# Optimization experiments

Hardware: AMD Instinct MI355X
Metric: run time of the kernel (lower is better)

Reference implementation:

```python
import jax, jax.numpy as jnp
import numpy as np

DIM = 512; DEPTH = 2; HEADS = 8; DIM_HEAD = 64; INNER = HEADS * DIM_HEAD
MEM = 16; TOPK = 8; FF = 4 * DIM
NUM_BUCKETS = 32; MAX_DIST = 128
EPS = 1e-5


def _layernorm(x, g, b):
    m = jnp.mean(x, axis=-1, keepdims=True)
    v = jnp.var(x, axis=-1, keepdims=True)
    return (x - m) * jax.lax.rsqrt(v + EPS) * g + b


def _rel_bucket(rel_pos):
    # T5 relative-position bucketing, causal=True (as hardcoded in Encoder)
    num_buckets = NUM_BUCKETS // 2  # 16
    n = -rel_pos
    ret = (n < 0).astype(jnp.int32) * num_buckets
    n = jnp.abs(n)
    max_exact = num_buckets // 2  # 8
    is_small = n < max_exact
    nf = jnp.maximum(n, 1).astype(jnp.float32)  # safe log; masked by is_small where n==0
    val_if_large = max_exact + (
        jnp.log(nf / max_exact) / np.log(MAX_DIST / max_exact) * (num_buckets - max_exact)
    ).astype(jnp.int32)
    val_if_large = jnp.minimum(val_if_large, num_buckets - 1)
    return ret + jnp.where(is_small, n, val_if_large)


def setup_inputs() -> dict:
    key = jax.random.key(0)
    ks = jax.random.split(key, 16)
    B, N = 2, 2048
    w = lambda k, shape, s=0.02: jax.random.normal(k, shape, jnp.float32) * s
    return {
        "x": jax.random.normal(ks[0], (B, N, DIM), jnp.float32),
        "ln1_g": jnp.ones((DEPTH, DIM), jnp.float32),
        "ln1_b": jnp.zeros((DEPTH, DIM), jnp.float32),
        "Wq": w(ks[1], (DEPTH, DIM, INNER)),
        "Wkv": w(ks[2], (DEPTH, DIM, 2 * INNER)),
        "Wo": w(ks[3], (DEPTH, INNER, DIM)),
        "bo": jnp.zeros((DEPTH, DIM), jnp.float32),
        "pre_proj": w(ks[4], (DEPTH, HEADS, HEADS), 1.0),  # torch.randn init
        "mem_k": w(ks[5], (DEPTH, HEADS, MEM, DIM_HEAD), 1.0),
        "mem_v": w(ks[6], (DEPTH, HEADS, MEM, DIM_HEAD), 1.0),
        "ln2_g": jnp.ones((DEPTH, DIM), jnp.float32),
        "ln2_b": jnp.zeros((DEPTH, DIM), jnp.float32),
        "W1": w(ks[7], (DEPTH, DIM, FF)),
        "b1": jnp.zeros((DEPTH, FF), jnp.float32),
        "W2": w(ks[8], (DEPTH, FF, DIM)),
        "b2": jnp.zeros((DEPTH, DIM), jnp.float32),
        "rel_emb": w(ks[9], (NUM_BUCKETS, HEADS)),
    }


def reference(x, ln1_g, ln1_b, Wq, Wkv, Wo, bo, pre_proj, mem_k, mem_v,
              ln2_g, ln2_b, W1, b1, W2, b2, rel_emb):
    B, N, _ = x.shape
    J = N + MEM  # keys include num_mem_kv memory slots
    scale = DIM_HEAD ** -0.5
    # relative position bias, shape (1, H, N, J); same for every layer
    rel = jnp.arange(J)[None, :] - jnp.arange(N)[:, None]
    bias = jnp.transpose(rel_emb[_rel_bucket(rel)], (2, 0, 1))[None]

    for l in range(DEPTH):
        # --- PreNorm(Attention) + residual ---
        h = _layernorm(x, ln1_g[l], ln1_b[l])
        q = (h @ Wq[l]).reshape(B, N, HEADS, DIM_HEAD).transpose(0, 2, 1, 3)
        k, v = jnp.split(h @ Wkv[l], 2, axis=-1)
        k = k.reshape(B, N, HEADS, DIM_HEAD).transpose(0, 2, 1, 3)
        v = v.reshape(B, N, HEADS, DIM_HEAD).transpose(0, 2, 1, 3)
        k = jnp.concatenate([jnp.broadcast_to(mem_k[l], (B, HEADS, MEM, DIM_HEAD)), k], axis=2)
        v = jnp.concatenate([jnp.broadcast_to(mem_v[l], (B, HEADS, MEM, DIM_HEAD)), v], axis=2)
        dots = jnp.einsum('bhid,bhjd->bhij', q, k) * scale
        dots = jnp.einsum('bhij,hk->bkij', dots, pre_proj[l])  # talking heads (pre-softmax)
        dots = dots + bias
        # sparse top-k masking: keep only values >= k-th largest per row
        thr = jax.lax.top_k(dots, TOPK)[0][..., -1:]
        dots = jnp.where(dots < thr, -jnp.inf, dots)
        attn = jax.nn.softmax(dots, axis=-1)
        out = jnp.einsum('bhij,bhjd->bhid', attn, v)
        out = out.transpose(0, 2, 1, 3).reshape(B, N, INNER)
        x = out @ Wo[l] + bo[l] + x
        # --- PreNorm(FeedForward) + residual ---
        h2 = _layernorm(x, ln2_g[l], ln2_b[l])
        x = jax.nn.gelu(h2 @ W1[l] + b1[l], approximate=False) @ W2[l] + b2[l] + x
    return x
```

## Files before the change

### kernel.cpp

```cpp
#include <hip/hip_runtime.h>
#include <cmath>

typedef __bf16 bf16;
typedef __attribute__((ext_vector_type(8))) __bf16 bf16x8;
typedef __attribute__((ext_vector_type(4))) __bf16 bf16x4;
typedef __attribute__((ext_vector_type(4))) float f32x4;

#define NB 2
#define NSEQ 2048
#define NDIM 512
#define NHEADS 8
#define DHEAD 64
#define NMEM 16
#define NJ 2064
#define NJP 2176
#define NFF 2048
#define NROWS (NB*NSEQ)
#define TBL 4111

enum { EPI_QKV = 0, EPI_GELUSPLIT = 1, EPI_RESID = 2 };

template<int BM, int BN, int WAVES_M, int WAVES_N, int EPI>
__global__ __launch_bounds__(256)
void gemm_split(const bf16* __restrict__ A, const bf16* __restrict__ B,
                void* __restrict__ Cv, const float* __restrict__ bias,
                void* __restrict__ Cv2, void* __restrict__ Cv3,
                int K, int lda, int ldb, int ldc, int loA, int loB)
{
  constexpr int BK = 32;
  constexpr int WM = BM / WAVES_M;
  constexpr int WN = BN / WAVES_N;
  constexpr int MF = WM / 16;
  constexpr int NF = WN / 16;
  constexpr int AI = (BM * BK * 2) / 4096;
  constexpr int BI = (BN * BK * 2) / 4096;
  __shared__ bf16 Ash[2][BM * BK];
  __shared__ bf16 Asl[2][BM * BK];
  __shared__ bf16 Bsh[2][BN * BK];
  __shared__ bf16 Bsl[2][BN * BK];

  const int bm0 = blockIdx.x * BM;
  const int bn0 = blockIdx.y * BN;
  const int t = threadIdx.x;
  const int wave = t >> 6, lane = t & 63;
  const int wr = wave / WAVES_N, wc = wave % WAVES_N;
  const int sr = t >> 2, sc = t & 3;
  const int frow = lane & 15, fk = (lane >> 4) * 8;

  auto stage = [&](int buf, int k0) {
#pragma unroll
    for (int qi = 0; qi < AI; ++qi) {
      const long long ro = (long long)(bm0 + qi * 64 + sr) * lda + (k0 + sc * 8);
      __builtin_amdgcn_global_load_lds(
          (const __attribute__((address_space(1))) void*)(A + ro),
          (__attribute__((address_space(3))) void*)(&Ash[buf][qi * 2048 + wave * 512]), 16, 0, 0);
      __builtin_amdgcn_global_load_lds(
          (const __attribute__((address_space(1))) void*)(A + ro + loA),
          (__attribute__((address_space(3))) void*)(&Asl[buf][qi * 2048 + wave * 512]), 16, 0, 0);
    }
#pragma unroll
    for (int qi = 0; qi < BI; ++qi) {
      const long long ro = (long long)(bn0 + qi * 64 + sr) * ldb + (k0 + sc * 8);
      __builtin_amdgcn_global_load_lds(
          (const __attribute__((address_space(1))) void*)(B + ro),
          (__attribute__((address_space(3))) void*)(&Bsh[buf][qi * 2048 + wave * 512]), 16, 0, 0);
      __builtin_amdgcn_global_load_lds(
          (const __attribute__((address_space(1))) void*)(B + ro + loB),
          (__attribute__((address_space(3))) void*)(&Bsl[buf][qi * 2048 + wave * 512]), 16, 0, 0);
    }
  };

  f32x4 acc[MF][NF] = {};

  stage(0, 0);
  __syncthreads();
  int cur = 0;
  for (int k0 = 0; k0 < K; k0 += BK) {
    if (k0 + BK < K) stage(cur ^ 1, k0 + BK);
    bf16x8 afh[MF], afl[MF], bfh[NF], bfl[NF];
#pragma unroll
    for (int m = 0; m < MF; m++) {
      afh[m] = *(const bf16x8*)(&Ash[cur][(wr * WM + m * 16 + frow) * BK + fk]);
      afl[m] = *(const bf16x8*)(&Asl[cur][(wr * WM + m * 16 + frow) * BK + fk]);
    }
#pragma unroll
    for (int n = 0; n < NF; n++) {
      bfh[n] = *(const bf16x8*)(&Bsh[cur][(wc * WN + n * 16 + frow) * BK + fk]);
      bfl[n] = *(const bf16x8*)(&Bsl[cur][(wc * WN + n * 16 + frow) * BK + fk]);
    }
#pragma unroll
    for (int m = 0; m < MF; m++)
#pragma unroll
      for (int n = 0; n < NF; n++) {
        acc[m][n] = __builtin_amdgcn_mfma_f32_16x16x32_bf16(afh[m], bfh[n], acc[m][n], 0, 0, 0);
        acc[m][n] = __builtin_amdgcn_mfma_f32_16x16x32_bf16(afl[m], bfh[n], acc[m][n], 0, 0, 0);
        acc[m][n] = __builtin_amdgcn_mfma_f32_16x16x32_bf16(afh[m], bfl[n], acc[m][n], 0, 0, 0);
      }
    __syncthreads();
    cur ^= 1;
  }

#pragma unroll
  for (int m = 0; m < MF; m++) {
#pragma unroll
    for (int n = 0; n < NF; n++) {
      const int row0 = bm0 + wr * WM + m * 16 + (lane >> 4) * 4;
      const int col = bn0 + wc * WN + n * 16 + (lane & 15);
#pragma unroll
      for (int r = 0; r < 4; r++) {
        const float v = acc[m][n][r];
        const long long i = row0 + r;
        if (EPI == EPI_QKV) {
          const int bb = (int)(i >> 11);
          const int il = (int)(i & 2047);
          if (col < NDIM) {
            const float vq = v * 0.125f;
            bf16* base = (bf16*)Cv;
            const long long ih = i * (long long)(2 * NDIM) + col;
            bf16 h = (bf16)vq;
            base[ih] = h;
            base[ih + NDIM] = (bf16)(vq - (float)h);
          } else if (col < 2 * NDIM) {
            bf16* ks = (bf16*)Cv3;
            const long long ih = ((long long)bb * NJP + il + NMEM) * (long long)(2 * NDIM)
                               + (col - NDIM);
            bf16 h = (bf16)v;
            ks[ih] = h;
            ks[ih + NDIM] = (bf16)(v - (float)h);
          } else {
            ((float*)Cv2)[i * (long long)NDIM + (col - 2 * NDIM)] = v;
          }
        } else if (EPI == EPI_GELUSPLIT) {
          float u = v + bias[col];
          float gl = 0.5f * u * (1.0f + erff(u * 0.7071067811865476f));
          const long long ih = i * (long long)(2 * ldc) + col;
          bf16 h = (bf16)gl;
          ((bf16*)Cv)[ih] = h;
          ((bf16*)Cv)[ih + ldc] = (bf16)(gl - (float)h);
        } else {
          float* xp = ((float*)Cv) + i * ldc + col;
          *xp = *xp + v + bias[col];
        }
      }
    }
  }
}

__global__ __launch_bounds__(256)
void s_gemm_direct(const bf16* __restrict__ Qs, const bf16* __restrict__ Ks,
                   float* __restrict__ S)
{
  const int h = blockIdx.z;
  const int bm0 = blockIdx.x * 128;
  const int bn0 = blockIdx.y * 128;
  const int t = threadIdx.x;
  const int wave = t >> 6, lane = t & 63;
  const int wr = wave >> 1, wc = wave & 1;
  const int frow = lane & 15, fk = (lane >> 4) * 8;

  bf16x8 ah[4][2], al[4][2];
#pragma unroll
  for (int m = 0; m < 4; m++)
#pragma unroll
    for (int kk = 0; kk < 2; kk++) {
      const bf16* ap = Qs + (long long)(bm0 + wr * 64 + m * 16 + frow) * 1024
                     + h * 64 + kk * 32 + fk;
      ah[m][kk] = *(const bf16x8*)(ap);
      al[m][kk] = *(const bf16x8*)(ap + 512);
    }

  f32x4 acc[4][4] = {};
#pragma unroll
  for (int n = 0; n < 4; n++) {
    bf16x8 bh[2], bl[2];
#pragma unroll
    for (int kk = 0; kk < 2; kk++) {
      const bf16* bp = Ks + (long long)(bn0 + wc * 64 + n * 16 + frow) * 1024
                     + h * 64 + kk * 32 + fk;
      bh[kk] = *(const bf16x8*)(bp);
      bl[kk] = *(const bf16x8*)(bp + 512);
    }
#pragma unroll
    for (int m = 0; m < 4; m++)
#pragma unroll
      for (int kk = 0; kk < 2; kk++) {
        acc[m][n] = __builtin_amdgcn_mfma_f32_16x16x32_bf16(ah[m][kk], bh[kk], acc[m][n], 0, 0, 0);
        acc[m][n] = __builtin_amdgcn_mfma_f32_16x16x32_bf16(al[m][kk], bh[kk], acc[m][n], 0, 0, 0);
        acc[m][n] = __builtin_amdgcn_mfma_f32_16x16x32_bf16(ah[m][kk], bl[kk], acc[m][n], 0, 0, 0);
      }
  }

#pragma unroll
  for (int m = 0; m < 4; m++) {
#pragma unroll
    for (int n = 0; n < 4; n++) {
      const int row0 = bm0 + wr * 64 + m * 16 + (lane >> 4) * 4;
      const int col = bn0 + wc * 64 + n * 16 + (lane & 15);
#pragma unroll
      for (int r = 0; r < 4; r++)
        S[(long long)(row0 + r) * (NHEADS * NJP) + h * NJP + col] = acc[m][n][r];
    }
  }
}

__global__ __launch_bounds__(256)
void ln_kernel(const float* __restrict__ x, const float* __restrict__ g,
               const float* __restrict__ b, bf16* __restrict__ out)
{
  const int row = blockIdx.x * 4 + (threadIdx.x >> 6);
  const int lane = threadIdx.x & 63;
  const float* xr = x + (long long)row * NDIM;
  float4 a0 = ((const float4*)xr)[lane];
  float4 a1 = ((const float4*)xr)[lane + 64];
  float s = a0.x + a0.y + a0.z + a0.w + a1.x + a1.y + a1.z + a1.w;
  float ss = a0.x * a0.x + a0.y * a0.y + a0.z * a0.z + a0.w * a0.w
           + a1.x * a1.x + a1.y * a1.y + a1.z * a1.z + a1.w * a1.w;
#pragma unroll
  for (int d = 1; d < 64; d <<= 1) {
    s += __shfl_xor(s, d, 64);
    ss += __shfl_xor(ss, d, 64);
  }
  const float mean = s * (1.0f / NDIM);
  const float var = ss * (1.0f / NDIM) - mean * mean;
  const float rs = rsqrtf(var + 1e-5f);
  float4 g0 = ((const float4*)g)[lane], g1 = ((const float4*)g)[lane + 64];
  float4 b0 = ((const float4*)b)[lane], b1 = ((const float4*)b)[lane + 64];
  bf16* orow = out + (long long)row * (2 * NDIM);
  float y[8] = {
    (a0.x - mean) * rs * g0.x + b0.x, (a0.y - mean) * rs * g0.y + b0.y,
    (a0.z - mean) * rs * g0.z + b0.z, (a0.w - mean) * rs * g0.w + b0.w,
    (a1.x - mean) * rs * g1.x + b1.x, (a1.y - mean) * rs * g1.y + b1.y,
    (a1.z - mean) * rs * g1.z + b1.z, (a1.w - mean) * rs * g1.w + b1.w };
  bf16x4 h0, h1, l0, l1;
#pragma unroll
  for (int j = 0; j < 4; j++) {
    bf16 h = (bf16)y[j];      h0[j] = h;  l0[j] = (bf16)(y[j] - (float)h);
    bf16 h2 = (bf16)y[4 + j]; h1[j] = h2; l1[j] = (bf16)(y[4 + j] - (float)h2);
  }
  *(bf16x4*)(orow + lane * 4) = h0;
  *(bf16x4*)(orow + 256 + lane * 4) = h1;
  *(bf16x4*)(orow + 512 + lane * 4) = l0;
  *(bf16x4*)(orow + 768 + lane * 4) = l1;
}

__global__ __launch_bounds__(256)
void ks_edges(const float* __restrict__ mem_k_l, bf16* __restrict__ Ks)
{
  const int idx = blockIdx.x * 256 + threadIdx.x;
  const int c = idx & 511;
  const int jj = (idx >> 9) & 127;
  const int bb = idx >> 16;
  const int j = (jj < NMEM) ? jj : (jj - NMEM + NJ);
  float kval = 0.f;
  if (jj < NMEM) kval = mem_k_l[((c >> 6) * NMEM + jj) * DHEAD + (c & 63)];
  bf16 hv = (bf16)kval;
  const long long ro = ((long long)bb * NJP + j) * (2 * NDIM) + c;
  Ks[ro] = hv;
  Ks[ro + NDIM] = (bf16)(kval - (float)hv);
}

__global__ __launch_bounds__(512)
void mix_topk_gather(const float* __restrict__ S, const float* __restrict__ kvV,
                     const float* __restrict__ mem_v_l, const float* __restrict__ pp,
                     const float* __restrict__ table2, bf16* __restrict__ obufs,
                     int b)
{
  const int i = blockIdx.x;
  const int k = threadIdx.x >> 6;
  const int lane = threadIdx.x & 63;
  const float* srow = S + (long long)i * (NHEADS * NJP);

  float pk[8];
#pragma unroll
  for (int h = 0; h < 8; h++) pk[h] = pp[h * 8 + k];
  const float* t2k = table2 + k * TBL + (2047 - i);

  float v[34];
#pragma unroll
  for (int t = 0; t < 8; t++) {
    const int j0 = 256 * t + 4 * lane;
    v[4 * t + 0] = t2k[j0];
    v[4 * t + 1] = t2k[j0 + 1];
    v[4 * t + 2] = t2k[j0 + 2];
    v[4 * t + 3] = t2k[j0 + 3];
  }
  {
    const int j0 = 2048 + 2 * lane;
    const int jc = j0 < 2062 ? j0 : 2062;
    v[32] = t2k[jc];
    v[33] = t2k[jc + 1];
  }

#pragma unroll
  for (int h = 0; h < 8; h++) {
    const float* sp = srow + h * NJP;
    const float w = pk[h];
#pragma unroll
    for (int t = 0; t < 8; t++) {
      const float4 s4 = *(const float4*)(sp + 256 * t + 4 * lane);
      v[4 * t + 0] = fmaf(s4.x, w, v[4 * t + 0]);
      v[4 * t + 1] = fmaf(s4.y, w, v[4 * t + 1]);
      v[4 * t + 2] = fmaf(s4.z, w, v[4 * t + 2]);
      v[4 * t + 3] = fmaf(s4.w, w, v[4 * t + 3]);
    }
    const float2 s2 = *(const float2*)(sp + 2048 + 2 * lane);
    v[32] = fmaf(s2.x, w, v[32]);
    v[33] = fmaf(s2.y, w, v[33]);
  }
  {
    const int j0 = 2048 + 2 * lane;
    if (j0 >= NJ) v[32] = -1e30f;
    if (j0 + 1 >= NJ) v[33] = -1e30f;
  }

  float t8[8];
#pragma unroll
  for (int m = 0; m < 8; m++) t8[m] = -3.0e38f;
#pragma unroll
  for (int e = 0; e < 34; e++) {
    float x = v[e];
#pragma unroll
    for (int m = 0; m < 8; m++) {
      const float hi = fmaxf(t8[m], x);
      x = fminf(t8[m], x);
      t8[m] = hi;
    }
  }

#pragma unroll
  for (int d = 1; d < 64; d <<= 1) {
    float o[8], m8[8];
#pragma unroll
    for (int m = 0; m < 8; m++) o[m] = __shfl_xor(t8[m], d, 64);
#pragma unroll
    for (int m = 0; m < 8; m++) m8[m] = fmaxf(t8[m], o[7 - m]);
#define CX(a, bq) { float hi = fmaxf(m8[a], m8[bq]); float lo = fminf(m8[a], m8[bq]); m8[a] = hi; m8[bq] = lo; }
    CX(0, 4) CX(1, 5) CX(2, 6) CX(3, 7)
    CX(0, 2) CX(1, 3) CX(4, 6) CX(5, 7)
    CX(0, 1) CX(2, 3) CX(4, 5) CX(6, 7)
#undef CX
#pragma unroll
    for (int m = 0; m < 8; m++) t8[m] = m8[m];
  }
  const float mx = t8[0];
  const float thr = t8[7];
  float denom = 0.f;
#pragma unroll
  for (int m = 0; m < 8; m++) denom += __expf(t8[m] - mx);
  const float inv = 1.0f / denom;

  float acc = 0.f;
#pragma unroll
  for (int t = 0; t < 8; t++) {
#pragma unroll
    for (int e = 0; e < 4; e++) {
      unsigned long long mball = __ballot(v[t * 4 + e] >= thr);
      while (mball) {
        const int l = __builtin_ctzll(mball);
        mball &= mball - 1;
        const int jj = 256 * t + 4 * l + e;
        const float sv = __shfl(v[t * 4 + e], l);
        const float w = __expf(sv - mx) * inv;
        const float vv = (jj < NMEM)
            ? mem_v_l[(k * NMEM + jj) * DHEAD + lane]
            : kvV[(long long)(b * NSEQ + (jj - NMEM)) * NDIM + k * DHEAD + lane];
        acc = fmaf(w, vv, acc);
      }
    }
  }
#pragma unroll
  for (int e = 0; e < 2; e++) {
    unsigned long long mball = __ballot(v[32 + e] >= thr);
    while (mball) {
      const int l = __builtin_ctzll(mball);
      mball &= mball - 1;
      const int jj = 2048 + 2 * l + e;
      const float sv = __shfl(v[32 + e], l);
      const float w = __expf(sv - mx) * inv;
      const float vv = (jj < NMEM)
          ? mem_v_l[(k * NMEM + jj) * DHEAD + lane]
          : kvV[(long long)(b * NSEQ + (jj - NMEM)) * NDIM + k * DHEAD + lane];
      acc = fmaf(w, vv, acc);
    }
  }

  const long long orow = (long long)(b * NSEQ + i) * (2 * NDIM) + k * DHEAD + lane;
  bf16 h = (bf16)acc;
  obufs[orow] = h;
  obufs[orow + NDIM] = (bf16)(acc - (float)h);
}

__global__ __launch_bounds__(256)
void transpose_split(const float* __restrict__ in, bf16* __restrict__ out,
                     int R, int C)
{
  const long long idx = (long long)blockIdx.x * 256 + threadIdx.x;
  if (idx >= (long long)R * C) return;
  const int r = (int)(idx / C);
  const int c = (int)(idx % C);
  float v = in[idx];
  bf16 h = (bf16)v;
  out[(long long)c * (2 * R) + r] = h;
  out[(long long)c * (2 * R) + R + r] = (bf16)(v - (float)h);
}

__global__ __launch_bounds__(256)
void build_bias2(const float* __restrict__ rel_emb, float* __restrict__ table2)
{
  const int idx = blockIdx.x * 256 + threadIdx.x;
  if (idx >= 8 * TBL) return;
  const int k = idx / TBL;
  const int rel = (idx % TBL) - 2047;
  const int n = -rel;
  const int ret = (n < 0) ? 16 : 0;
  const int na = n < 0 ? -n : n;
  int bucket;
  if (na < 8) {
    bucket = ret + na;
  } else {
    int vl = 8 + (int)(log2((double)na * 0.125) * 2.0);
    vl = vl < 15 ? vl : 15;
    bucket = ret + vl;
  }
  table2[idx] = rel_emb[bucket * 8 + k];
}

extern "C" void kernel_launch(void* const* d_in, const int* in_sizes, int n_in,
                              void* d_out, int out_size, void* d_ws, size_t ws_size,
                              hipStream_t stream)
{
  const float* x_in    = (const float*)d_in[0];
  const float* ln1_g   = (const float*)d_in[1];
  const float* ln1_b   = (const float*)d_in[2];
  const float* Wq      = (const float*)d_in[3];
  const float* Wkv     = (const float*)d_in[4];
  const float* Wo      = (const float*)d_in[5];
  const float* bo      = (const float*)d_in[6];
  const float* pre_proj= (const float*)d_in[7];
  const float* mem_k   = (const float*)d_in[8];
  const float* mem_v   = (const float*)d_in[9];
  const float* ln2_g   = (const float*)d_in[10];
  const float* ln2_b   = (const float*)d_in[11];
  const float* W1      = (const float*)d_in[12];
  const float* b1      = (const float*)d_in[13];
  const float* W2      = (const float*)d_in[14];
  const float* b2      = (const float*)d_in[15];
  const float* rel_emb = (const float*)d_in[16];

  char* p = (char*)d_ws;
  auto alloc = [&](size_t bytes) -> char* {
    char* r = p;
    p += (bytes + 255) & ~(size_t)255;
    return r;
  };

  float* x    = (float*)alloc((size_t)NROWS * NDIM * 4);
  char*  RA   = alloc((size_t)NROWS * 2 * NDIM * 2);
  bf16*  hs    = (bf16*)RA;
  bf16*  obufs = (bf16*)RA;
  char*  RB   = alloc((size_t)NROWS * 2 * NFF * 2);
  bf16*  Qs    = (bf16*)RB;
  bf16*  Ks    = (bf16*)(RB + (size_t)NROWS * 2 * NDIM * 2);
  bf16*  tbufs = (bf16*)RB;
  float* kvV  = (float*)alloc((size_t)NROWS * NDIM * 4);
  float* S    = (float*)alloc((size_t)NSEQ * NHEADS * NJP * 4);
  bf16*  WqkvT= (bf16*)alloc((size_t)2 * 3 * NDIM * 2 * NDIM * 2);
  bf16*  WoT  = (bf16*)alloc((size_t)2 * NDIM * 2 * NDIM * 2);
  bf16*  W1T  = (bf16*)alloc((size_t)2 * NFF * 2 * NDIM * 2);
  bf16*  W2T  = (bf16*)alloc((size_t)2 * NDIM * 2 * NFF * 2);
  float* table2= (float*)alloc((size_t)8 * TBL * 4);

  hipMemcpyAsync(x, x_in, (size_t)NROWS * NDIM * 4, hipMemcpyDeviceToDevice, stream);
  build_bias2<<<(8 * TBL + 255) / 256, 256, 0, stream>>>(rel_emb, table2);
  for (int l = 0; l < 2; l++) {
    bf16* WqkvT_l = WqkvT + (size_t)l * 3 * NDIM * 2 * NDIM;
    transpose_split<<<(NDIM * NDIM + 255) / 256, 256, 0, stream>>>(
        Wq + (size_t)l * NDIM * NDIM, WqkvT_l, NDIM, NDIM);
    transpose_split<<<(2 * NDIM * NDIM + 255) / 256, 256, 0, stream>>>(
        Wkv + (size_t)l * NDIM * 2 * NDIM, WqkvT_l + (size_t)NDIM * 2 * NDIM,
        NDIM, 2 * NDIM);
    transpose_split<<<(NDIM * NDIM + 255) / 256, 256, 0, stream>>>(
        Wo + (size_t)l * NDIM * NDIM, WoT + (size_t)l * NDIM * 2 * NDIM, NDIM, NDIM);
    transpose_split<<<(NDIM * NFF + 255) / 256, 256, 0, stream>>>(
        W1 + (size_t)l * NDIM * NFF, W1T + (size_t)l * NFF * 2 * NDIM, NDIM, NFF);
    transpose_split<<<(NFF * NDIM + 255) / 256, 256, 0, stream>>>(
        W2 + (size_t)l * NFF * NDIM, W2T + (size_t)l * NDIM * 2 * NFF, NFF, NDIM);
  }

  for (int l = 0; l < 2; l++) {
    const bf16* WqkvT_l = WqkvT + (size_t)l * 3 * NDIM * 2 * NDIM;
    const bf16* WoT_l  = WoT + (size_t)l * NDIM * 2 * NDIM;
    const bf16* W1T_l  = W1T + (size_t)l * NFF * 2 * NDIM;
    const bf16* W2T_l  = W2T + (size_t)l * NDIM * 2 * NFF;
    const float* mem_v_l = mem_v + (size_t)l * NHEADS * NMEM * DHEAD;

    ln_kernel<<<NROWS / 4, 256, 0, stream>>>(x, ln1_g + l * NDIM, ln1_b + l * NDIM, hs);
    gemm_split<128, 128, 2, 2, EPI_QKV><<<dim3(NROWS / 128, 12), 256, 0, stream>>>(
        hs, WqkvT_l, Qs, nullptr, kvV, Ks, NDIM, 2 * NDIM, 2 * NDIM, 0, NDIM, NDIM);
    ks_edges<<<(2 * 128 * 512) / 256, 256, 0, stream>>>(
        mem_k + (size_t)l * NHEADS * NMEM * DHEAD, Ks);

    for (int b = 0; b < NB; b++) {
      s_gemm_direct<<<dim3(NSEQ / 128, NJP / 128, NHEADS), 256, 0, stream>>>(
          Qs + (long long)b * NSEQ * 1024, Ks + (long long)b * NJP * 1024, S);
      mix_topk_gather<<<NSEQ, 512, 0, stream>>>(
          S, kvV, mem_v_l, pre_proj + l * 64, table2, obufs, b);
    }

    gemm_split<128, 64, 2, 2, EPI_RESID><<<dim3(NROWS / 128, NDIM / 64), 256, 0, stream>>>(
        obufs, WoT_l, x, bo + l * NDIM, nullptr, nullptr,
        NDIM, 2 * NDIM, 2 * NDIM, NDIM, NDIM, NDIM);

    ln_kernel<<<NROWS / 4, 256, 0, stream>>>(x, ln2_g + l * NDIM, ln2_b + l * NDIM, hs);
    gemm_split<128, 128, 2, 2, EPI_GELUSPLIT><<<dim3(NROWS / 128, NFF / 128), 256, 0, stream>>>(
        hs, W1T_l, tbufs, b1 + l * NFF, nullptr, nullptr,
        NDIM, 2 * NDIM, 2 * NDIM, NFF, NDIM, NDIM);
    gemm_split<128, 64, 2, 2, EPI_RESID><<<dim3(NROWS / 128, NDIM / 64), 256, 0, stream>>>(
        tbufs, W2T_l, x, b2 + l * NDIM, nullptr, nullptr,
        NFF, 2 * NFF, 2 * NFF, NDIM, NFF, NFF);
  }

  hipMemcpyAsync(d_out, x, (size_t)out_size * 4, hipMemcpyDeviceToDevice, stream);
}
```

Measured before the change: 881.7 us.

## Split top-k attention into partitioned candidate selection and merge-gather kernels

The fused mix/top-k/gather kernel, which processed a full 2064-key row per block, is replaced by two kernels. The first splits each row into four 544-key slices, computes the talking-heads mix plus bias, and writes per-slice top-8 candidates. The second merges the 32 candidates per head and does the softmax-weighted V gather. The aim is more parallelism and lower register pressure per block, at the cost of an extra launch and a round trip of the candidates through global memory.

```diff
diff --git a/kernel.cpp b/kernel.cpp
--- a/kernel.cpp
+++ b/kernel.cpp
@@ -17,6 +17,7 @@
 #define NFF 2048
 #define NROWS (NB*NSEQ)
 #define TBL 4111
+#define JSL 544
 
 enum { EPI_QKV = 0, EPI_GELUSPLIT = 1, EPI_RESID = 2 };
 
@@ -260,64 +261,55 @@
 }
 
 __global__ __launch_bounds__(512)
-void mix_topk_gather(const float* __restrict__ S, const float* __restrict__ kvV,
-                     const float* __restrict__ mem_v_l, const float* __restrict__ pp,
-                     const float* __restrict__ table2, bf16* __restrict__ obufs,
-                     int b)
-{
-  const int i = blockIdx.x;
+void mix_part(const float* __restrict__ S, const float* __restrict__ pp,
+              const float* __restrict__ table2,
+              float* __restrict__ cand_v, int* __restrict__ cand_i)
+{
+  const int i  = blockIdx.x;
+  const int jb = blockIdx.y;
   const int k = threadIdx.x >> 6;
   const int lane = threadIdx.x & 63;
-  const float* srow = S + (long long)i * (NHEADS * NJP);
+  const int base = jb * JSL;
+  const float* srow = S + (long long)i * (NHEADS * NJP) + base;
 
   float pk[8];
 #pragma unroll
   for (int h = 0; h < 8; h++) pk[h] = pp[h * 8 + k];
   const float* t2k = table2 + k * TBL + (2047 - i);
 
-  float v[34];
-#pragma unroll
-  for (int t = 0; t < 8; t++) {
-    const int j0 = 256 * t + 4 * lane;
-    v[4 * t + 0] = t2k[j0];
-    v[4 * t + 1] = t2k[j0 + 1];
-    v[4 * t + 2] = t2k[j0 + 2];
-    v[4 * t + 3] = t2k[j0 + 3];
-  }
-  {
-    const int j0 = 2048 + 2 * lane;
-    const int jc = j0 < 2062 ? j0 : 2062;
-    v[32] = t2k[jc];
-    v[33] = t2k[jc + 1];
+  float v[12];
+#pragma unroll
+  for (int e = 0; e < 12; e++) {
+    const int jl = (e < 4) ? 4 * lane + e
+                 : (e < 8) ? 256 + 4 * lane + (e - 4)
+                           : 512 + 4 * lane + (e - 8);
+    const bool live = (e < 8) || (lane < 8);
+    const int j = base + jl;
+    v[e] = (live && j < NJ) ? t2k[j] : -1e30f;
   }
 
 #pragma unroll
   for (int h = 0; h < 8; h++) {
     const float* sp = srow + h * NJP;
     const float w = pk[h];
-#pragma unroll
-    for (int t = 0; t < 8; t++) {
-      const float4 s4 = *(const float4*)(sp + 256 * t + 4 * lane);
-      v[4 * t + 0] = fmaf(s4.x, w, v[4 * t + 0]);
-      v[4 * t + 1] = fmaf(s4.y, w, v[4 * t + 1]);
-      v[4 * t + 2] = fmaf(s4.z, w, v[4 * t + 2]);
-      v[4 * t + 3] = fmaf(s4.w, w, v[4 * t + 3]);
-    }
-    const float2 s2 = *(const float2*)(sp + 2048 + 2 * lane);
-    v[32] = fmaf(s2.x, w, v[32]);
-    v[33] = fmaf(s2.y, w, v[33]);
-  }
-  {
-    const int j0 = 2048 + 2 * lane;
-    if (j0 >= NJ) v[32] = -1e30f;
-    if (j0 + 1 >= NJ) v[33] = -1e30f;
+    const float4 a = *(const float4*)(sp + 4 * lane);
+    const float4 b2 = *(const float4*)(sp + 256 + 4 * lane);
+    v[0] = fmaf(a.x, w, v[0]);  v[1] = fmaf(a.y, w, v[1]);
+    v[2] = fmaf(a.z, w, v[2]);  v[3] = fmaf(a.w, w, v[3]);
+    v[4] = fmaf(b2.x, w, v[4]); v[5] = fmaf(b2.y, w, v[5]);
+    v[6] = fmaf(b2.z, w, v[6]); v[7] = fmaf(b2.w, w, v[7]);
+    if (lane < 8) {
+      const float4 c = *(const float4*)(sp + 512 + 4 * lane);
+      v[8] = fmaf(c.x, w, v[8]);  v[9] = fmaf(c.y, w, v[9]);
+      v[10] = fmaf(c.z, w, v[10]); v[11] = fmaf(c.w, w, v[11]);
+    }
   }
 
   float t8[8];
 #pragma unroll
   for (int m = 0; m < 8; m++) t8[m] = -3.0e38f;
 #pragma unroll
-  for (int e = 0; e < 34; e++) {
+  for (int e = 0; e < 12; e++) {
     float x = v[e];
 #pragma unroll
     for (int m = 0; m < 8; m++) {
@@ -342,6 +334,64 @@
 #pragma unroll
     for (int m = 0; m < 8; m++) t8[m] = m8[m];
   }
+  const float thr = t8[7];
+
+  const long long cbase = (((long long)i * NHEADS + k) * 32) + jb * 8;
+  int slot = 0;
+  for (int e = 0; e < 12; e++) {
+    if (slot >= 8) break;
+    unsigned long long mball = __ballot(v[e] >= thr);
+    while (mball && slot < 8) {
+      const int l = __builtin_ctzll(mball);
+      mball &= mball - 1;
+      if (lane == l) {
+        const int jl = (e < 4) ? 4 * lane + e
+                     : (e < 8) ? 256 + 4 * lane + (e - 4)
+                               : 512 + 4 * lane + (e - 8);
+        cand_v[cbase + slot] = v[e];
+        cand_i[cbase + slot] = base + jl;
+      }
+      slot++;
+    }
+  }
+}
+
+__global__ __launch_bounds__(512)
+void merge_gather(const float* __restrict__ cand_v, const int* __restrict__ cand_i,
+                  const float* __restrict__ kvV, const float* __restrict__ mem_v_l,
+                  bf16* __restrict__ obufs, int b)
+{
+  const int i = blockIdx.x;
+  const int k = threadIdx.x >> 6;
+  const int lane = threadIdx.x & 63;
+  const long long cbase = ((long long)i * NHEADS + k) * 32;
+
+  float cv = -3.0e38f;
+  int ci = 0;
+  if (lane < 32) {
+    cv = cand_v[cbase + lane];
+    ci = cand_i[cbase + lane];
+  }
+
+  float t8[8];
+  t8[0] = cv;
+#pragma unroll
+  for (int m = 1; m < 8; m++) t8[m] = -3.0e38f;
+#pragma unroll
+  for (int d = 1; d < 64; d <<= 1) {
+    float o[8], m8[8];
+#pragma unroll
+    for (int m = 0; m < 8; m++) o[m] = __shfl_xor(t8[m], d, 64);
+#pragma unroll
+    for (int m = 0; m < 8; m++) m8[m] = fmaxf(t8[m], o[7 - m]);
+#define CX(a, bq) { float hi = fmaxf(m8[a], m8[bq]); float lo = fminf(m8[a], m8[bq]); m8[a] = hi; m8[bq] = lo; }
+    CX(0, 4) CX(1, 5) CX(2, 6) CX(3, 7)
+    CX(0, 2) CX(1, 3) CX(4, 6) CX(5, 7)
+    CX(0, 1) CX(2, 3) CX(4, 5) CX(6, 7)
+#undef CX
+#pragma unroll
+    for (int m = 0; m < 8; m++) t8[m] = m8[m];
+  }
   const float mx = t8[0];
   const float thr = t8[7];
   float denom = 0.f;
@@ -350,38 +400,19 @@
   const float inv = 1.0f / denom;
 
   float acc = 0.f;
-#pragma unroll
-  for (int t = 0; t < 8; t++) {
-#pragma unroll
-    for (int e = 0; e < 4; e++) {
-      unsigned long long mball = __ballot(v[t * 4 + e] >= thr);
-      while (mball) {
-        const int l = __builtin_ctzll(mball);
-        mball &= mball - 1;
-        const int jj = 256 * t + 4 * l + e;
-        const float sv = __shfl(v[t * 4 + e], l);
-        const float w = __expf(sv - mx) * inv;
-        const float vv = (jj < NMEM)
-            ? mem_v_l[(k * NMEM + jj) * DHEAD + lane]
-            : kvV[(long long)(b * NSEQ + (jj - NMEM)) * NDIM + k * DHEAD + lane];
-        acc = fmaf(w, vv, acc);
-      }
-    }
-  }
-#pragma unroll
-  for (int e = 0; e < 2; e++) {
-    unsigned long long mball = __ballot(v[32 + e] >= thr);
-    while (mball) {
-      const int l = __builtin_ctzll(mball);
-      mball &= mball - 1;
-      const int jj = 2048 + 2 * l + e;
-      const float sv = __shfl(v[32 + e], l);
-      const float w = __expf(sv - mx) * inv;
-      const float vv = (jj < NMEM)
-          ? mem_v_l[(k * NMEM + jj) * DHEAD + lane]
-          : kvV[(long long)(b * NSEQ + (jj - NMEM)) * NDIM + k * DHEAD + lane];
-      acc = fmaf(w, vv, acc);
-    }
+  unsigned long long mball = __ballot(cv >= thr);
+  int cnt = 0;
+  while (mball && cnt < 8) {
+    const int l = __builtin_ctzll(mball);
+    mball &= mball - 1;
+    const int jj = __shfl(ci, l);
+    const float sv = __shfl(cv, l);
+    const float w = __expf(sv - mx) * inv;
+    const float vv = (jj < NMEM)
+        ? mem_v_l[(k * NMEM + jj) * DHEAD + lane]
+        : kvV[(long long)(b * NSEQ + (jj - NMEM)) * NDIM + k * DHEAD + lane];
+    acc = fmaf(w, vv, acc);
+    cnt++;
   }
 
   const long long orow = (long long)(b * NSEQ + i) * (2 * NDIM) + k * DHEAD + lane;
@@ -464,6 +495,8 @@
   bf16*  tbufs = (bf16*)RB;
   float* kvV  = (float*)alloc((size_t)NROWS * NDIM * 4);
   float* S    = (float*)alloc((size_t)NSEQ * NHEADS * NJP * 4);
+  float* cand_v = (float*)alloc((size_t)NSEQ * NHEADS * 32 * 4);
+  int*   cand_i = (int*)  alloc((size_t)NSEQ * NHEADS * 32 * 4);
   bf16*  WqkvT= (bf16*)alloc((size_t)2 * 3 * NDIM * 2 * NDIM * 2);
   bf16*  WoT  = (bf16*)alloc((size_t)2 * NDIM * 2 * NDIM * 2);
   bf16*  W1T  = (bf16*)alloc((size_t)2 * NFF * 2 * NDIM * 2);
@@ -503,8 +536,10 @@
     for (int b = 0; b < NB; b++) {
       s_gemm_direct<<<dim3(NSEQ / 128, NJP / 128, NHEADS), 256, 0, stream>>>(
           Qs + (long long)b * NSEQ * 1024, Ks + (long long)b * NJP * 1024, S);
-      mix_topk_gather<<<NSEQ, 512, 0, stream>>>(
-          S, kvV, mem_v_l, pre_proj + l * 64, table2, obufs, b);
+      mix_part<<<dim3(NSEQ, 4), 512, 0, stream>>>(
+          S, pre_proj + l * 64, table2, cand_v, cand_i);
+      merge_gather<<<NSEQ, 512, 0, stream>>>(
+          cand_v, cand_i, kvV, mem_v_l, obufs, b);
     }
 
     gemm_split<128, 64, 2, 2, EPI_RESID><<<dim3(NROWS / 128, NDIM / 64), 256, 0, stream>>>(
```

Measured after the change: 1.115 ms. +26.5%, slower.

## Split top-k across key halves and pair output heads per wave in mix kernel

Applied to the files above, without the earlier changes.

Rewrites the talking-heads mix plus top-k kernel so that each wave computes two output heads over half of the key range, instead of one head over all keys. Each S row load is reused for two heads, and per-wave register state shrinks from 34 to 17 values per head. Each half writes its local top-8 candidates to shared memory, and one wave per pair merges the 16 candidates and does the softmax and V gather. The cost is a block-wide sync and an extra merge step, and half the waves sit idle during the gather.

```diff
diff --git a/kernel.cpp b/kernel.cpp
--- a/kernel.cpp
+++ b/kernel.cpp
@@ -259,74 +259,8 @@
   Ks[ro + NDIM] = (bf16)(kval - (float)hv);
 }
 
-__global__ __launch_bounds__(512)
-void mix_topk_gather(const float* __restrict__ S, const float* __restrict__ kvV,
-                     const float* __restrict__ mem_v_l, const float* __restrict__ pp,
-                     const float* __restrict__ table2, bf16* __restrict__ obufs,
-                     int b)
-{
-  const int i = blockIdx.x;
-  const int k = threadIdx.x >> 6;
-  const int lane = threadIdx.x & 63;
-  const float* srow = S + (long long)i * (NHEADS * NJP);
-
-  float pk[8];
-#pragma unroll
-  for (int h = 0; h < 8; h++) pk[h] = pp[h * 8 + k];
-  const float* t2k = table2 + k * TBL + (2047 - i);
-
-  float v[34];
-#pragma unroll
-  for (int t = 0; t < 8; t++) {
-    const int j0 = 256 * t + 4 * lane;
-    v[4 * t + 0] = t2k[j0];
-    v[4 * t + 1] = t2k[j0 + 1];
-    v[4 * t + 2] = t2k[j0 + 2];
-    v[4 * t + 3] = t2k[j0 + 3];
-  }
-  {
-    const int j0 = 2048 + 2 * lane;
-    const int jc = j0 < 2062 ? j0 : 2062;
-    v[32] = t2k[jc];
-    v[33] = t2k[jc + 1];
-  }
-
-#pragma unroll
-  for (int h = 0; h < 8; h++) {
-    const float* sp = srow + h * NJP;
-    const float w = pk[h];
-#pragma unroll
-    for (int t = 0; t < 8; t++) {
-      const float4 s4 = *(const float4*)(sp + 256 * t + 4 * lane);
-      v[4 * t + 0] = fmaf(s4.x, w, v[4 * t + 0]);
-      v[4 * t + 1] = fmaf(s4.y, w, v[4 * t + 1]);
-      v[4 * t + 2] = fmaf(s4.z, w, v[4 * t + 2]);
-      v[4 * t + 3] = fmaf(s4.w, w, v[4 * t + 3]);
-    }
-    const float2 s2 = *(const float2*)(sp + 2048 + 2 * lane);
-    v[32] = fmaf(s2.x, w, v[32]);
-    v[33] = fmaf(s2.y, w, v[33]);
-  }
-  {
-    const int j0 = 2048 + 2 * lane;
-    if (j0 >= NJ) v[32] = -1e30f;
-    if (j0 + 1 >= NJ) v[33] = -1e30f;
-  }
-
-  float t8[8];
-#pragma unroll
-  for (int m = 0; m < 8; m++) t8[m] = -3.0e38f;
-#pragma unroll
-  for (int e = 0; e < 34; e++) {
-    float x = v[e];
-#pragma unroll
-    for (int m = 0; m < 8; m++) {
-      const float hi = fmaxf(t8[m], x);
-      x = fminf(t8[m], x);
-      t8[m] = hi;
-    }
-  }
-
+__device__ __forceinline__ void butterfly8(float t8[8])
+{
 #pragma unroll
   for (int d = 1; d < 64; d <<= 1) {
     float o[8], m8[8];
@@ -342,52 +276,164 @@
 #pragma unroll
     for (int m = 0; m < 8; m++) t8[m] = m8[m];
   }
-  const float mx = t8[0];
-  const float thr = t8[7];
-  float denom = 0.f;
-#pragma unroll
-  for (int m = 0; m < 8; m++) denom += __expf(t8[m] - mx);
-  const float inv = 1.0f / denom;
-
-  float acc = 0.f;
-#pragma unroll
-  for (int t = 0; t < 8; t++) {
-#pragma unroll
-    for (int e = 0; e < 4; e++) {
-      unsigned long long mball = __ballot(v[t * 4 + e] >= thr);
-      while (mball) {
+}
+
+__global__ __launch_bounds__(512)
+void mix_topk2(const float* __restrict__ S, const float* __restrict__ kvV,
+               const float* __restrict__ mem_v_l, const float* __restrict__ pp,
+               const float* __restrict__ table2, bf16* __restrict__ obufs,
+               int b)
+{
+  __shared__ float cv_s[NHEADS][16];
+  __shared__ int   ci_s[NHEADS][16];
+  const int i = blockIdx.x;
+  const int wv = threadIdx.x >> 6;
+  const int kp = wv >> 1;
+  const int jh = wv & 1;
+  const int lane = threadIdx.x & 63;
+  const int base = jh * 1088;
+  const float* srow = S + (long long)i * (NHEADS * NJP);
+  const int k0 = kp * 2, k1 = k0 + 1;
+
+  float pk0[8], pk1[8];
+#pragma unroll
+  for (int h = 0; h < 8; h++) {
+    pk0[h] = pp[h * 8 + k0];
+    pk1[h] = pp[h * 8 + k1];
+  }
+  const float* t0 = table2 + k0 * TBL + (2047 - i);
+  const float* t1 = table2 + k1 * TBL + (2047 - i);
+
+  float va[17], vb[17];
+#pragma unroll
+  for (int e = 0; e < 17; e++) {
+    const int jl = (e < 16) ? (256 * (e >> 2) + 4 * lane + (e & 3)) : (1024 + lane);
+    const int j = base + jl;
+    const bool valid = (j < NJ);
+    va[e] = valid ? t0[j] : -1e30f;
+    vb[e] = valid ? t1[j] : -1e30f;
+  }
+
+#pragma unroll
+  for (int h = 0; h < 8; h++) {
+    const float* sp = srow + h * NJP + base;
+    const float w0 = pk0[h], w1 = pk1[h];
+#pragma unroll
+    for (int t = 0; t < 4; t++) {
+      const float4 s4 = *(const float4*)(sp + 256 * t + 4 * lane);
+      va[4 * t + 0] = fmaf(s4.x, w0, va[4 * t + 0]);
+      va[4 * t + 1] = fmaf(s4.y, w0, va[4 * t + 1]);
+      va[4 * t + 2] = fmaf(s4.z, w0, va[4 * t + 2]);
+      va[4 * t + 3] = fmaf(s4.w, w0, va[4 * t + 3]);
+      vb[4 * t + 0] = fmaf(s4.x, w1, vb[4 * t + 0]);
+      vb[4 * t + 1] = fmaf(s4.y, w1, vb[4 * t + 1]);
+      vb[4 * t + 2] = fmaf(s4.z, w1, vb[4 * t + 2]);
+      vb[4 * t + 3] = fmaf(s4.w, w1, vb[4 * t + 3]);
+    }
+    const float st = sp[1024 + lane];
+    va[16] = fmaf(st, w0, va[16]);
+    vb[16] = fmaf(st, w1, vb[16]);
+  }
+
+  float ta[8], tb[8];
+#pragma unroll
+  for (int m = 0; m < 8; m++) { ta[m] = -3.0e38f; tb[m] = -3.0e38f; }
+#pragma unroll
+  for (int e = 0; e < 17; e++) {
+    float x = va[e];
+#pragma unroll
+    for (int m = 0; m < 8; m++) {
+      const float hi = fmaxf(ta[m], x);
+      x = fminf(ta[m], x);
+      ta[m] = hi;
+    }
+    float y = vb[e];
+#pragma unroll
+    for (int m = 0; m < 8; m++) {
+      const float hi = fmaxf(tb[m], y);
+      y = fminf(tb[m], y);
+      tb[m] = hi;
+    }
+  }
+  butterfly8(ta);
+  butterfly8(tb);
+  const float thra = ta[7];
+  const float thrb = tb[7];
+
+  {
+    int slot = 0;
+    for (int e = 0; e < 17; e++) {
+      if (slot >= 8) break;
+      unsigned long long mball = __ballot(va[e] >= thra);
+      while (mball && slot < 8) {
         const int l = __builtin_ctzll(mball);
         mball &= mball - 1;
-        const int jj = 256 * t + 4 * l + e;
-        const float sv = __shfl(v[t * 4 + e], l);
-        const float w = __expf(sv - mx) * inv;
-        const float vv = (jj < NMEM)
-            ? mem_v_l[(k * NMEM + jj) * DHEAD + lane]
-            : kvV[(long long)(b * NSEQ + (jj - NMEM)) * NDIM + k * DHEAD + lane];
-        acc = fmaf(w, vv, acc);
+        if (lane == l) {
+          const int jl = (e < 16) ? (256 * (e >> 2) + 4 * lane + (e & 3)) : (1024 + lane);
+          cv_s[k0][jh * 8 + slot] = va[e];
+          ci_s[k0][jh * 8 + slot] = base + jl;
+        }
+        slot++;
       }
     }
   }
-#pragma unroll
-  for (int e = 0; e < 2; e++) {
-    unsigned long long mball = __ballot(v[32 + e] >= thr);
+  {
+    int slot = 0;
+    for (int e = 0; e < 17; e++) {
+      if (slot >= 8) break;
+      unsigned long long mball = __ballot(vb[e] >= thrb);
+      while (mball && slot < 8) {
+        const int l = __builtin_ctzll(mball);
+        mball &= mball - 1;
+        if (lane == l) {
+          const int jl = (e < 16) ? (256 * (e >> 2) + 4 * lane + (e & 3)) : (1024 + lane);
+          cv_s[k1][jh * 8 + slot] = vb[e];
+          ci_s[k1][jh * 8 + slot] = base + jl;
+        }
+        slot++;
+      }
+    }
+  }
+  __syncthreads();
+
+  if (jh != 0) return;
+
+#pragma unroll
+  for (int kk = 0; kk < 2; kk++) {
+    const int k = k0 + kk;
+    float cv = (lane < 16) ? cv_s[k][lane] : -3.0e38f;
+    int ci = (lane < 16) ? ci_s[k][lane] : 0;
+    float t8[8];
+    t8[0] = cv;
+#pragma unroll
+    for (int m = 1; m < 8; m++) t8[m] = -3.0e38f;
+    butterfly8(t8);
+    const float mx = t8[0];
+    const float thr = t8[7];
+    float denom = 0.f;
+#pragma unroll
+    for (int m = 0; m < 8; m++) denom += __expf(t8[m] - mx);
+    const float inv = 1.0f / denom;
+
+    float acc = 0.f;
+    unsigned long long mball = __ballot(cv >= thr);
     while (mball) {
       const int l = __builtin_ctzll(mball);
       mball &= mball - 1;
-      const int jj = 2048 + 2 * l + e;
-      const float sv = __shfl(v[32 + e], l);
+      const int jj = __shfl(ci, l);
+      const float sv = __shfl(cv, l);
       const float w = __expf(sv - mx) * inv;
       const float vv = (jj < NMEM)
           ? mem_v_l[(k * NMEM + jj) * DHEAD + lane]
           : kvV[(long long)(b * NSEQ + (jj - NMEM)) * NDIM + k * DHEAD + lane];
       acc = fmaf(w, vv, acc);
     }
-  }
-
-  const long long orow = (long long)(b * NSEQ + i) * (2 * NDIM) + k * DHEAD + lane;
-  bf16 h = (bf16)acc;
-  obufs[orow] = h;
-  obufs[orow + NDIM] = (bf16)(acc - (float)h);
+
+    const long long orow = (long long)(b * NSEQ + i) * (2 * NDIM) + k * DHEAD + lane;
+    bf16 h = (bf16)acc;
+    obufs[orow] = h;
+    obufs[orow + NDIM] = (bf16)(acc - (float)h);
+  }
 }
 
 __global__ __launch_bounds__(256)
@@ -503,7 +549,7 @@
     for (int b = 0; b < NB; b++) {
       s_gemm_direct<<<dim3(NSEQ / 128, NJP / 128, NHEADS), 256, 0, stream>>>(
           Qs + (long long)b * NSEQ * 1024, Ks + (long long)b * NJP * 1024, S);
-      mix_topk_gather<<<NSEQ, 512, 0, stream>>>(
+      mix_topk2<<<NSEQ, 512, 0, stream>>>(
           S, kvV, mem_v_l, pre_proj + l * 64, table2, obufs, b);
     }
 
```

Result: slower. 1.006 ms (+14.1%).
